# Kernel tuning notes

Measured on AMD Instinct MI355X. Metric: run time of the kernel, lower is better.

Reference implementation:

```python
import jax, jax.numpy as jnp
import numpy as np

EPS = 1e-5          # InstanceNorm eps (torch default)
KERNEL = 25         # moving_avg_kernel_size
TAU = 1.0           # gumbel softmax temperature
REGIME_NUM = 8


def _inorm(x):
    # InstanceNorm1d without affine on (N, C, L): normalize over last dim (biased var)
    m = x.mean(-1, keepdims=True)
    v = ((x - m) ** 2).mean(-1, keepdims=True)
    return (x - m) * jax.lax.rsqrt(v + EPS)


def _lbr(x, W, b):
    # Linear -> InstanceNorm (over last dim) -> exact GELU
    return jax.nn.gelu(_inorm(x @ W + b), approximate=False)


def _moving_avg(x, k):
    # x: (B, L, C); edge-replicate pad (k-1)//2 on both sides, sliding mean via cumsum
    p = (k - 1) // 2
    xp = jnp.concatenate([jnp.repeat(x[:, :1], p, axis=1), x,
                          jnp.repeat(x[:, -1:], p, axis=1)], axis=1)
    cs = jnp.concatenate([jnp.zeros_like(xp[:, :1]), jnp.cumsum(xp, axis=1)], axis=1)
    return (cs[:, k:] - cs[:, :-k]) / k  # (B, L, C)


def _encode(x, Ws, bs, Wt, bt):
    # inputs - inputs[:, 0:1]; series decomposition; seasonal+trend branches
    x = x - x[:, :1]
    mm = _moving_avg(x, KERNEL)
    return _lbr(x - mm, Ws, bs) + _lbr(mm, Wt, bt)  # (B, L, H)


def reference(inputs_longterm, inputs_shortterm,
              Ws, bs, Wt, bt,
              Wh1, bh1, Wl1, bl1, Wh2, bh2, Wl2, bl2, Wh3, bh3, Wl3, bl3,
              Wr, br, proto):
    e_lt = _encode(inputs_longterm, Ws, bs, Wt, bt)   # (B, L_lt, H)
    e_st = _encode(inputs_shortterm, Ws, bs, Wt, bt)  # (B, L_st, H)

    # RegimeEncoder: alternate hidden-dim and lookback-dim LinearBatchRelu layers
    o = _lbr(e_lt, Wh1, bh1)
    o = jnp.swapaxes(_lbr(jnp.swapaxes(o, 1, 2), Wl1, bl1), 1, 2)
    o = _lbr(o, Wh2, bh2)
    o = jnp.swapaxes(_lbr(jnp.swapaxes(o, 1, 2), Wl2, bl2), 1, 2)
    o = _lbr(o, Wh3, bh3)
    o = jnp.swapaxes(_lbr(jnp.swapaxes(o, 1, 2), Wl3, bl3), 1, 2)  # (B, L_lt//8, H)
    logits = o.reshape(o.shape[0], -1) @ Wr + br  # (B, R)

    # gumbel_softmax(hard=True) with straight-through estimator
    g = jax.random.gumbel(jax.random.key(42), logits.shape, logits.dtype)
    y_soft = jax.nn.softmax((logits + g) / TAU, axis=-1)
    y_hard = jax.nn.one_hot(jnp.argmax(y_soft, axis=-1), REGIME_NUM, dtype=logits.dtype)
    w = y_hard - jax.lax.stop_gradient(y_soft) + y_soft  # (B, R)

    # weighted sum over regime prototypes, then combine with encoded shortterm
    sel = jnp.einsum('br,rnhmo->bnhmo', w, proto)          # (B, L_st, H, M, 3)
    out = jnp.einsum('bnh,bnhmo->bmo', e_st, sel)          # (B, M, 3)
    B = out.shape[0]
    return jax.nn.softmax(out.reshape(B, -1), axis=-1).reshape(out.shape)


def setup_inputs() -> dict:
    key = jax.random.key(0)
    ks = jax.random.split(key, 24)
    B, L_lt, L_st, C, H, R, M = 32, 512, 128, 9, 128, 8, 64
    s = 0.02
    d = {
        'inputs_longterm':  jax.random.normal(ks[0], (B, L_lt, C), jnp.float32),
        'inputs_shortterm': jax.random.normal(ks[1], (B, L_st, C), jnp.float32),
        'Ws': jax.random.normal(ks[2], (C, H), jnp.float32) * s,
        'bs': jnp.zeros((H,), jnp.float32),
        'Wt': jax.random.normal(ks[3], (C, H), jnp.float32) * s,
        'bt': jnp.zeros((H,), jnp.float32),
        'Wh1': jax.random.normal(ks[4], (H, H), jnp.float32) * s,
        'bh1': jnp.zeros((H,), jnp.float32),
        'Wl1': jax.random.normal(ks[5], (L_lt, L_lt // 2), jnp.float32) * s,
        'bl1': jnp.zeros((L_lt // 2,), jnp.float32),
        'Wh2': jax.random.normal(ks[6], (H, H), jnp.float32) * s,
        'bh2': jnp.zeros((H,), jnp.float32),
        'Wl2': jax.random.normal(ks[7], (L_lt // 2, L_lt // 4), jnp.float32) * s,
        'bl2': jnp.zeros((L_lt // 4,), jnp.float32),
        'Wh3': jax.random.normal(ks[8], (H, H), jnp.float32) * s,
        'bh3': jnp.zeros((H,), jnp.float32),
        'Wl3': jax.random.normal(ks[9], (L_lt // 4, L_lt // 8), jnp.float32) * s,
        'bl3': jnp.zeros((L_lt // 8,), jnp.float32),
        'Wr': jax.random.normal(ks[10], (H * L_lt // 8, R), jnp.float32) * s,
        'br': jnp.zeros((R,), jnp.float32),
        'proto': jax.random.normal(ks[11], (R, L_st, H, M, 3), jnp.float32),
    }
    return d
```

## Files before the change

### kernel.cpp

```cpp
#include <hip/hip_runtime.h>
#include <math.h>

#define EPS 1e-5f

__device__ __forceinline__ float gelu_exact(float x) {
    return 0.5f * x * (1.0f + erff(x * 0.7071067811865476f));
}

__device__ float block_sum(float v, float* red) {
    int lane = threadIdx.x & 63, wid = threadIdx.x >> 6;
#pragma unroll
    for (int off = 32; off > 0; off >>= 1) v += __shfl_down(v, off, 64);
    if (lane == 0) red[wid] = v;
    __syncthreads();
    int nw = ((int)blockDim.x + 63) >> 6;
    float s = red[0];
    for (int w = 1; w < nw; w++) s += red[w];
    __syncthreads();
    return s;
}

__device__ float block_max(float v, float* red) {
    int lane = threadIdx.x & 63, wid = threadIdx.x >> 6;
#pragma unroll
    for (int off = 32; off > 0; off >>= 1) v = fmaxf(v, __shfl_down(v, off, 64));
    if (lane == 0) red[wid] = v;
    __syncthreads();
    int nw = ((int)blockDim.x + 63) >> 6;
    float s = red[0];
    for (int w = 1; w < nw; w++) s = fmaxf(s, red[w]);
    __syncthreads();
    return s;
}

__device__ void threefry2x32(unsigned k0, unsigned k1, unsigned x0, unsigned x1,
                             unsigned& o0, unsigned& o1) {
    unsigned ks[3] = {k0, k1, k0 ^ k1 ^ 0x1BD11BDAu};
    const unsigned rot[2][4] = {{13u, 15u, 26u, 6u}, {17u, 29u, 16u, 24u}};
    x0 += ks[0]; x1 += ks[1];
#pragma unroll
    for (int i = 0; i < 5; i++) {
#pragma unroll
        for (int j = 0; j < 4; j++) {
            unsigned r = rot[i & 1][j];
            x0 += x1;
            x1 = (x1 << r) | (x1 >> (32 - r));
            x1 ^= x0;
        }
        x0 += ks[(i + 1) % 3];
        x1 += ks[(i + 2) % 3] + (unsigned)(i + 1);
    }
    o0 = x0; o1 = x1;
}

__device__ float gumbel_at(int j) {
    unsigned o0, o1;
    threefry2x32(0u, 42u, 0u, (unsigned)j, o0, o1);
    unsigned bits = o0 ^ o1;
    float f = __uint_as_float((bits >> 9) | 0x3F800000u) - 1.0f;
    float u = fmaxf(f + 1.17549435e-38f, 1.17549435e-38f);
    return -logf(-logf(u));
}

__device__ void bsum2_128(float& a, float& b, float (*red)[2]) {
    int lane = threadIdx.x & 63, wid = threadIdx.x >> 6;
#pragma unroll
    for (int off = 32; off > 0; off >>= 1) {
        a += __shfl_xor(a, off, 64);
        b += __shfl_xor(b, off, 64);
    }
    if (lane == 0) { red[wid][0] = a; red[wid][1] = b; }
    __syncthreads();
    a = red[0][0] + red[1][0];
    b = red[0][1] + red[1][1];
}

__global__ void encode_kernel(const float* __restrict__ x_lt, const float* __restrict__ x_st,
                              const float* __restrict__ Ws, const float* __restrict__ bs,
                              const float* __restrict__ Wt, const float* __restrict__ bt,
                              float* __restrict__ e_lt, float* __restrict__ e_st) {
    const int H = 128;
    int b = blockIdx.y, t = threadIdx.x;
    const float* x;
    float* e;
    int L, l;
    if (blockIdx.x < 512) { x = x_lt; e = e_lt; L = 512; l = blockIdx.x; }
    else { x = x_st; e = e_st; L = 128; l = blockIdx.x - 512; }
    __shared__ float part[117];
    __shared__ float seas[9], mmv[9];
    __shared__ float redA[2][2], redB[2][2];
    const float* xb = x + (size_t)b * L * 9;
    if (t < 117) {
        int c = t / 13, g = t % 13;
        int lj0 = l + 2 * g - 12;
        lj0 = lj0 < 0 ? 0 : (lj0 >= L ? L - 1 : lj0);
        float s = xb[(size_t)lj0 * 9 + c];
        if (g < 12) {
            int lj1 = l + 2 * g - 11;
            lj1 = lj1 < 0 ? 0 : (lj1 >= L ? L - 1 : lj1);
            s += xb[(size_t)lj1 * 9 + c];
        }
        part[t] = s;
    }
    __syncthreads();
    if (t < 9) {
        float s = 0.f;
        for (int g = 0; g < 13; g++) s += part[t * 13 + g];
        float x0 = xb[t];
        float mm = (s - 25.f * x0) * (1.0f / 25.0f);
        float xd = xb[(size_t)l * 9 + t] - x0;
        mmv[t] = mm;
        seas[t] = xd - mm;
    }
    __syncthreads();
    float ys = bs[t], yt = bt[t];
#pragma unroll
    for (int c = 0; c < 9; c++) {
        ys += seas[c] * Ws[c * H + t];
        yt += mmv[c] * Wt[c * H + t];
    }
    float sa = ys, sb = yt;
    bsum2_128(sa, sb, redA);
    float ms = sa * (1.0f / 128.0f), mt = sb * (1.0f / 128.0f);
    float ds = ys - ms, dt = yt - mt;
    float qa = ds * ds, qb = dt * dt;
    bsum2_128(qa, qb, redB);
    float gy = gelu_exact(ds * rsqrtf(qa * (1.0f / 128.0f) + EPS));
    float gt = gelu_exact(dt * rsqrtf(qb * (1.0f / 128.0f) + EPS));
    e[((size_t)b * L + l) * H + t] = gy + gt;
}

template <int K, int N, int WR, bool TRANS>
__global__ __launch_bounds__(256) void lbr_wave(
    const float* __restrict__ A, int S, int ABOFF,
    const float* __restrict__ W, const float* __restrict__ bias,
    float* __restrict__ out, int OROWS, int OBOFF) {
    constexpr int CG = N / 4;
    constexpr int SG = 64 / CG;
    constexpr int RW = SG * WR;
    constexpr int MT = 4 * RW;
    constexpr int LOG2MT = (MT == 8) ? 3 : ((MT == 16) ? 4 : 5);
    constexpr int STAGE = 4 * RW * K;
    constexpr int TILE = TRANS ? MT * (N + 4) : 0;
    constexpr int LSZ = STAGE > TILE ? STAGE : TILE;
    __shared__ float lds[LSZ];
    const int t = threadIdx.x;
    const int w = t >> 6, ln = t & 63;
    const int sg = ln / CG;
    const int n0 = (ln % CG) * 4;
    const int b = blockIdx.y;
    const int r0b = blockIdx.x * MT;
    const int r0w = r0b + w * RW;
    float* As = lds + w * RW * K;
    const float* Ab = A + (size_t)b * ABOFF;
    for (int idx = ln; idx < RW * (K / 4); idx += 64) {
        int rr = idx / (K / 4), kk = idx % (K / 4);
        float4 v = *(const float4*)(Ab + (size_t)(r0w + rr) * S + kk * 4);
        *(float4*)(As + rr * K + kk * 4) = v;
    }
    float4 acc[WR];
    {
        float4 bv = *(const float4*)(bias + n0);
#pragma unroll
        for (int j = 0; j < WR; j++) acc[j] = bv;
    }
    const float* ap = As + (sg * WR) * K;
    const float* wp = W + n0;
#pragma unroll 2
    for (int k = 0; k < K; k += 4) {
        float4 w0 = *(const float4*)(wp);
        float4 w1 = *(const float4*)(wp + N);
        float4 w2 = *(const float4*)(wp + 2 * N);
        float4 w3 = *(const float4*)(wp + 3 * N);
        wp += 4 * N;
#pragma unroll
        for (int j = 0; j < WR; j++) {
            float4 a4 = *(const float4*)(ap + j * K + k);
            acc[j].x += a4.x * w0.x; acc[j].y += a4.x * w0.y;
            acc[j].z += a4.x * w0.z; acc[j].w += a4.x * w0.w;
            acc[j].x += a4.y * w1.x; acc[j].y += a4.y * w1.y;
            acc[j].z += a4.y * w1.z; acc[j].w += a4.y * w1.w;
            acc[j].x += a4.z * w2.x; acc[j].y += a4.z * w2.y;
            acc[j].z += a4.z * w2.z; acc[j].w += a4.z * w2.w;
            acc[j].x += a4.w * w3.x; acc[j].y += a4.w * w3.y;
            acc[j].z += a4.w * w3.z; acc[j].w += a4.w * w3.w;
        }
    }
    float4 res[WR];
#pragma unroll
    for (int j = 0; j < WR; j++) {
        float s = acc[j].x + acc[j].y + acc[j].z + acc[j].w;
#pragma unroll
        for (int off = CG / 2; off > 0; off >>= 1) s += __shfl_xor(s, off, 64);
        float m = s * (1.0f / (float)N);
        float dx = acc[j].x - m, dy = acc[j].y - m, dz = acc[j].z - m, dw = acc[j].w - m;
        float q = dx * dx + dy * dy + dz * dz + dw * dw;
#pragma unroll
        for (int off = CG / 2; off > 0; off >>= 1) q += __shfl_xor(q, off, 64);
        float inv = rsqrtf(q * (1.0f / (float)N) + EPS);
        res[j].x = gelu_exact(dx * inv);
        res[j].y = gelu_exact(dy * inv);
        res[j].z = gelu_exact(dz * inv);
        res[j].w = gelu_exact(dw * inv);
    }
    if constexpr (TRANS) {
        __syncthreads();
#pragma unroll
        for (int j = 0; j < WR; j++) {
            int rl = w * RW + sg * WR + j;
            *(float4*)(lds + rl * (N + 4) + n0) = res[j];
        }
        __syncthreads();
        float* ob = out + (size_t)b * OBOFF + r0b;
        for (int e = t; e < MT * N; e += 256) {
            int r = e & (MT - 1), n = e >> LOG2MT;
            ob[(size_t)n * OROWS + r] = lds[r * (N + 4) + n];
        }
    } else {
        float* ob = out + (size_t)b * OBOFF;
#pragma unroll
        for (int j = 0; j < WR; j++) {
            int row = r0w + sg * WR + j;
            *(float4*)(ob + (size_t)row * N + n0) = res[j];
        }
    }
}

__global__ __launch_bounds__(256) void logits_select(
    const float* __restrict__ O6, const float* __restrict__ Wr,
    const float* __restrict__ br, float* __restrict__ sel_w, int* __restrict__ sel_r) {
    int b = blockIdx.x, t = threadIdx.x;
    __shared__ float sO6[128 * 68];
    __shared__ float red[4][8];
    const float4* ob4 = (const float4*)(O6 + (size_t)b * 8192);
    for (int i4 = t; i4 < 2048; i4 += 256) {
        float4 v = ob4[i4];
        int p = i4 * 4;
        int h = p >> 6, l4 = p & 63;
        *(float4*)(&sO6[h * 68 + l4]) = v;
    }
    __syncthreads();
    float acc[8] = {0, 0, 0, 0, 0, 0, 0, 0};
#pragma unroll 4
    for (int q = 0; q < 32; q++) {
        int i = q * 256 + t;
        int l4 = i >> 7, h = i & 127;
        float v = sO6[h * 68 + l4];
        const float4* wr = (const float4*)(Wr + (size_t)i * 8);
        float4 w0 = wr[0], w1 = wr[1];
        acc[0] += v * w0.x; acc[1] += v * w0.y; acc[2] += v * w0.z; acc[3] += v * w0.w;
        acc[4] += v * w1.x; acc[5] += v * w1.y; acc[6] += v * w1.z; acc[7] += v * w1.w;
    }
#pragma unroll
    for (int j = 0; j < 8; j++)
#pragma unroll
        for (int off = 32; off > 0; off >>= 1) acc[j] += __shfl_xor(acc[j], off, 64);
    int lane = t & 63, wid = t >> 6;
    if (lane == 0)
        for (int j = 0; j < 8; j++) red[wid][j] = acc[j];
    __syncthreads();
    if (t == 0) {
        float z[8];
        for (int j = 0; j < 8; j++) {
            float lg = br[j] + red[0][j] + red[1][j] + red[2][j] + red[3][j];
            z[j] = lg + gumbel_at(b * 8 + j);
        }
        int am = 0;
        float zm = z[0];
        for (int j = 1; j < 8; j++)
            if (z[j] > zm) { zm = z[j]; am = j; }
        float ssum = 0.f;
        for (int j = 0; j < 8; j++) ssum += expf(z[j] - zm);
        float s = 1.0f / ssum;
        sel_w[b] = (1.0f - s) + s;
        sel_r[b] = am;
    }
}

__global__ void einsum_nsplit(const float* __restrict__ e_st, const float* __restrict__ proto,
                              const int* __restrict__ sel_r, float* __restrict__ part) {
    int n = blockIdx.x, r = blockIdx.y, t = threadIdx.x;
    __shared__ int loc[32];
    __shared__ int s_gs;
    if (t == 0) {
        int g = 0;
        for (int bb = 0; bb < 32; bb++)
            if (sel_r[bb] == r) loc[g++] = bb;
        s_gs = g;
    }
    __syncthreads();
    int gs = s_gs;
    if (gs == 0) return;
    __shared__ float es[8][128];
    const float* pb = proto + ((size_t)r * 128 + n) * 128 * 192;
    for (int s0 = 0; s0 < gs; s0 += 8) {
        int np = gs - s0 < 8 ? gs - s0 : 8;
        __syncthreads();
        for (int i4 = t; i4 < 256; i4 += 192) {
            int sb = i4 >> 5, h4 = i4 & 31;
            float4 v = make_float4(0.f, 0.f, 0.f, 0.f);
            if (sb < np) {
                int b = loc[s0 + sb];
                v = ((const float4*)(e_st + ((size_t)b * 128 + n) * 128))[h4];
            }
            *(float4*)(&es[sb][h4 * 4]) = v;
        }
        __syncthreads();
        float a0 = 0.f, a1 = 0.f, a2 = 0.f, a3 = 0.f;
        float a4 = 0.f, a5 = 0.f, a6 = 0.f, a7 = 0.f;
#pragma unroll 8
        for (int h = 0; h < 128; h++) {
            float p = pb[h * 192 + t];
            a0 += es[0][h] * p; a1 += es[1][h] * p;
            a2 += es[2][h] * p; a3 += es[3][h] * p;
            a4 += es[4][h] * p; a5 += es[5][h] * p;
            a6 += es[6][h] * p; a7 += es[7][h] * p;
        }
        float av[8] = {a0, a1, a2, a3, a4, a5, a6, a7};
#pragma unroll
        for (int sb = 0; sb < 8; sb++) {
            if (sb < np) {
                int b = loc[s0 + sb];
                part[((size_t)b * 128 + n) * 192 + t] = av[sb];
            }
        }
    }
}

__global__ void finalize_kernel(const float* __restrict__ part, const float* __restrict__ sel_w,
                                float* __restrict__ out) {
    int b = blockIdx.x, t = threadIdx.x;
    __shared__ float red[4];
    float v = 0.f;
#pragma unroll 8
    for (int c = 0; c < 128; c++) v += part[((size_t)b * 128 + c) * 192 + t];
    v *= sel_w[b];
    float mx = block_max(v, red);
    float e = expf(v - mx);
    float s = block_sum(e, red);
    out[(size_t)b * 192 + t] = e / s;
}

extern "C" void kernel_launch(void* const* d_in, const int* in_sizes, int n_in,
                              void* d_out, int out_size, void* d_ws, size_t ws_size,
                              hipStream_t stream) {
    const float* in_lt = (const float*)d_in[0];
    const float* in_st = (const float*)d_in[1];
    const float* Ws  = (const float*)d_in[2];  const float* bs  = (const float*)d_in[3];
    const float* Wt  = (const float*)d_in[4];  const float* bt  = (const float*)d_in[5];
    const float* Wh1 = (const float*)d_in[6];  const float* bh1 = (const float*)d_in[7];
    const float* Wl1 = (const float*)d_in[8];  const float* bl1 = (const float*)d_in[9];
    const float* Wh2 = (const float*)d_in[10]; const float* bh2 = (const float*)d_in[11];
    const float* Wl2 = (const float*)d_in[12]; const float* bl2 = (const float*)d_in[13];
    const float* Wh3 = (const float*)d_in[14]; const float* bh3 = (const float*)d_in[15];
    const float* Wl3 = (const float*)d_in[16]; const float* bl3 = (const float*)d_in[17];
    const float* Wr  = (const float*)d_in[18]; const float* br  = (const float*)d_in[19];
    const float* proto = (const float*)d_in[20];
    float* out = (float*)d_out;

    float* ws = (float*)d_ws;
    size_t off = 0;
    float* e_lt = ws + off; off += (size_t)32 * 512 * 128;
    float* e_st = ws + off; off += (size_t)32 * 128 * 128;
    float* O1T = ws + off; off += (size_t)128 * 16384;
    float* O2T = ws + off; off += (size_t)256 * 4096;
    float* O3T = ws + off; off += (size_t)128 * 8192;
    float* O4T = ws + off; off += (size_t)128 * 4096;
    float* O5T = ws + off; off += (size_t)128 * 4096;
    float* O6 = ws + off; off += (size_t)32 * 128 * 64;
    float* part = ws + off; off += (size_t)32 * 128 * 192;
    float* sel_w = ws + off; off += 32;
    int* sel_r = (int*)(ws + off); off += 32;

    encode_kernel<<<dim3(640, 32), 128, 0, stream>>>(in_lt, in_st, Ws, bs, Wt, bt, e_lt, e_st);
    lbr_wave<128, 128, 2, true><<<dim3(1024, 1), 256, 0, stream>>>(
        e_lt, 128, 0, Wh1, bh1, O1T, 16384, 0);
    lbr_wave<512, 256, 2, true><<<dim3(16, 32), 256, 0, stream>>>(
        O1T, 16384, 512, Wl1, bl1, O2T, 4096, 128);
    lbr_wave<128, 128, 2, true><<<dim3(16, 32), 256, 0, stream>>>(
        O2T, 4096, 128, Wh2, bh2, O3T, 8192, 256);
    lbr_wave<256, 128, 1, true><<<dim3(16, 32), 256, 0, stream>>>(
        O3T, 8192, 256, Wl2, bl2, O4T, 4096, 128);
    lbr_wave<128, 128, 1, true><<<dim3(16, 32), 256, 0, stream>>>(
        O4T, 4096, 128, Wh3, bh3, O5T, 4096, 128);
    lbr_wave<128, 64, 1, false><<<dim3(8, 32), 256, 0, stream>>>(
        O5T, 4096, 128, Wl3, bl3, O6, 0, 8192);
    logits_select<<<32, 256, 0, stream>>>(O6, Wr, br, sel_w, sel_r);
    einsum_nsplit<<<dim3(128, 8), 192, 0, stream>>>(e_st, proto, sel_r, part);
    finalize_kernel<<<32, 192, 0, stream>>>(part, sel_w, out);
}
```

Baseline: 362.2 us.

## Fuse all stages into one persistent cooperative kernel with grid syncs

Replaces the ten separate kernel launches with a single cooperative persistent kernel of 512 blocks that walks every stage in grid-stride loops and separates stages with grid.sync(). The encode stage is also rewritten so each wave handles one row, using shuffles instead of shared memory and block barriers. The aim is to remove per-launch overhead and the inter-kernel gaps on a pipeline of many small stages. In exchange it adds grid-wide barrier cost, and occupancy is capped by the shared-memory footprint of the largest stage and by launch_bounds(256,2).

```diff
diff --git a/kernel.cpp b/kernel.cpp
--- a/kernel.cpp
+++ b/kernel.cpp
@@ -1,36 +1,13 @@
 #include <hip/hip_runtime.h>
+#include <hip/hip_cooperative_groups.h>
 #include <math.h>
+
+namespace cg = cooperative_groups;
 
 #define EPS 1e-5f
 
 __device__ __forceinline__ float gelu_exact(float x) {
     return 0.5f * x * (1.0f + erff(x * 0.7071067811865476f));
-}
-
-__device__ float block_sum(float v, float* red) {
-    int lane = threadIdx.x & 63, wid = threadIdx.x >> 6;
-#pragma unroll
-    for (int off = 32; off > 0; off >>= 1) v += __shfl_down(v, off, 64);
-    if (lane == 0) red[wid] = v;
-    __syncthreads();
-    int nw = ((int)blockDim.x + 63) >> 6;
-    float s = red[0];
-    for (int w = 1; w < nw; w++) s += red[w];
-    __syncthreads();
-    return s;
-}
-
-__device__ float block_max(float v, float* red) {
-    int lane = threadIdx.x & 63, wid = threadIdx.x >> 6;
-#pragma unroll
-    for (int off = 32; off > 0; off >>= 1) v = fmaxf(v, __shfl_down(v, off, 64));
-    if (lane == 0) red[wid] = v;
-    __syncthreads();
-    int nw = ((int)blockDim.x + 63) >> 6;
-    float s = red[0];
-    for (int w = 1; w < nw; w++) s = fmaxf(s, red[w]);
-    __syncthreads();
-    return s;
 }
 
 __device__ void threefry2x32(unsigned k0, unsigned k1, unsigned x0, unsigned x1,
@@ -62,330 +39,349 @@
     return -logf(-logf(u));
 }
 
-__device__ void bsum2_128(float& a, float& b, float (*red)[2]) {
-    int lane = threadIdx.x & 63, wid = threadIdx.x >> 6;
-#pragma unroll
-    for (int off = 32; off > 0; off >>= 1) {
-        a += __shfl_xor(a, off, 64);
-        b += __shfl_xor(b, off, 64);
-    }
-    if (lane == 0) { red[wid][0] = a; red[wid][1] = b; }
-    __syncthreads();
-    a = red[0][0] + red[1][0];
-    b = red[0][1] + red[1][1];
-}
-
-__global__ void encode_kernel(const float* __restrict__ x_lt, const float* __restrict__ x_st,
-                              const float* __restrict__ Ws, const float* __restrict__ bs,
-                              const float* __restrict__ Wt, const float* __restrict__ bt,
-                              float* __restrict__ e_lt, float* __restrict__ e_st) {
-    const int H = 128;
-    int b = blockIdx.y, t = threadIdx.x;
+struct MegaParams {
+    const float *in_lt, *in_st;
+    const float *Ws, *bs, *Wt, *bt;
+    const float *Wh1, *bh1, *Wl1, *bl1, *Wh2, *bh2, *Wl2, *bl2;
+    const float *Wh3, *bh3, *Wl3, *bl3, *Wr, *br, *proto;
+    float* out;
+    float *e_lt, *e_st, *O1T, *O2T, *O3T, *O4T, *O5T, *O6, *part, *sel_w;
+    int* sel_r;
+};
+
+__device__ void encode_row_wave(int task, const MegaParams& p, int ln) {
     const float* x;
     float* e;
-    int L, l;
-    if (blockIdx.x < 512) { x = x_lt; e = e_lt; L = 512; l = blockIdx.x; }
-    else { x = x_st; e = e_st; L = 128; l = blockIdx.x - 512; }
-    __shared__ float part[117];
-    __shared__ float seas[9], mmv[9];
-    __shared__ float redA[2][2], redB[2][2];
+    int L, b, l;
+    if (task < 16384) { x = p.in_lt; e = p.e_lt; L = 512; b = task >> 9; l = task & 511; }
+    else { int u = task - 16384; x = p.in_st; e = p.e_st; L = 128; b = u >> 7; l = u & 127; }
     const float* xb = x + (size_t)b * L * 9;
-    if (t < 117) {
-        int c = t / 13, g = t % 13;
-        int lj0 = l + 2 * g - 12;
-        lj0 = lj0 < 0 ? 0 : (lj0 >= L ? L - 1 : lj0);
-        float s = xb[(size_t)lj0 * 9 + c];
-        if (g < 12) {
-            int lj1 = l + 2 * g - 11;
-            lj1 = lj1 < 0 ? 0 : (lj1 >= L ? L - 1 : lj1);
-            s += xb[(size_t)lj1 * 9 + c];
-        }
-        part[t] = s;
-    }
-    __syncthreads();
-    if (t < 9) {
+    float seas_v = 0.f, mm_v = 0.f;
+    if (ln < 9) {
+        float x0 = xb[ln];
         float s = 0.f;
-        for (int g = 0; g < 13; g++) s += part[t * 13 + g];
-        float x0 = xb[t];
+#pragma unroll
+        for (int j = -12; j <= 12; j++) {
+            int lj = l + j;
+            lj = lj < 0 ? 0 : (lj >= L ? L - 1 : lj);
+            s += xb[(size_t)lj * 9 + ln];
+        }
         float mm = (s - 25.f * x0) * (1.0f / 25.0f);
-        float xd = xb[(size_t)l * 9 + t] - x0;
-        mmv[t] = mm;
-        seas[t] = xd - mm;
-    }
-    __syncthreads();
-    float ys = bs[t], yt = bt[t];
+        mm_v = mm;
+        seas_v = (xb[(size_t)l * 9 + ln] - x0) - mm;
+    }
+    int h1 = ln, h2 = ln + 64;
+    float ys1 = p.bs[h1], ys2 = p.bs[h2], yt1 = p.bt[h1], yt2 = p.bt[h2];
 #pragma unroll
     for (int c = 0; c < 9; c++) {
-        ys += seas[c] * Ws[c * H + t];
-        yt += mmv[c] * Wt[c * H + t];
-    }
-    float sa = ys, sb = yt;
-    bsum2_128(sa, sb, redA);
+        float sc = __shfl(seas_v, c, 64);
+        float mc = __shfl(mm_v, c, 64);
+        ys1 += sc * p.Ws[c * 128 + h1]; ys2 += sc * p.Ws[c * 128 + h2];
+        yt1 += mc * p.Wt[c * 128 + h1]; yt2 += mc * p.Wt[c * 128 + h2];
+    }
+    float sa = ys1 + ys2, sb = yt1 + yt2;
+#pragma unroll
+    for (int off = 32; off > 0; off >>= 1) {
+        sa += __shfl_xor(sa, off, 64);
+        sb += __shfl_xor(sb, off, 64);
+    }
     float ms = sa * (1.0f / 128.0f), mt = sb * (1.0f / 128.0f);
-    float ds = ys - ms, dt = yt - mt;
-    float qa = ds * ds, qb = dt * dt;
-    bsum2_128(qa, qb, redB);
-    float gy = gelu_exact(ds * rsqrtf(qa * (1.0f / 128.0f) + EPS));
-    float gt = gelu_exact(dt * rsqrtf(qb * (1.0f / 128.0f) + EPS));
-    e[((size_t)b * L + l) * H + t] = gy + gt;
+    float d1 = ys1 - ms, d2 = ys2 - ms, f1 = yt1 - mt, f2 = yt2 - mt;
+    float qa = d1 * d1 + d2 * d2, qb = f1 * f1 + f2 * f2;
+#pragma unroll
+    for (int off = 32; off > 0; off >>= 1) {
+        qa += __shfl_xor(qa, off, 64);
+        qb += __shfl_xor(qb, off, 64);
+    }
+    float is = rsqrtf(qa * (1.0f / 128.0f) + EPS);
+    float it = rsqrtf(qb * (1.0f / 128.0f) + EPS);
+    float o1 = gelu_exact(d1 * is) + gelu_exact(f1 * it);
+    float o2 = gelu_exact(d2 * is) + gelu_exact(f2 * it);
+    float* eb = e + ((size_t)b * L + l) * 128;
+    eb[h1] = o1;
+    eb[h2] = o2;
 }
 
 template <int K, int N, int WR, bool TRANS>
-__global__ __launch_bounds__(256) void lbr_wave(
-    const float* __restrict__ A, int S, int ABOFF,
-    const float* __restrict__ W, const float* __restrict__ bias,
-    float* __restrict__ out, int OROWS, int OBOFF) {
+__device__ void layer_phase(float* lds,
+                            const float* __restrict__ A, int S, int ABOFF,
+                            const float* __restrict__ W, const float* __restrict__ bias,
+                            float* __restrict__ out, int OROWS, int OBOFF,
+                            int tilesX, int nB) {
     constexpr int CG = N / 4;
     constexpr int SG = 64 / CG;
     constexpr int RW = SG * WR;
     constexpr int MT = 4 * RW;
     constexpr int LOG2MT = (MT == 8) ? 3 : ((MT == 16) ? 4 : 5);
-    constexpr int STAGE = 4 * RW * K;
-    constexpr int TILE = TRANS ? MT * (N + 4) : 0;
-    constexpr int LSZ = STAGE > TILE ? STAGE : TILE;
-    __shared__ float lds[LSZ];
     const int t = threadIdx.x;
     const int w = t >> 6, ln = t & 63;
     const int sg = ln / CG;
     const int n0 = (ln % CG) * 4;
-    const int b = blockIdx.y;
-    const int r0b = blockIdx.x * MT;
-    const int r0w = r0b + w * RW;
-    float* As = lds + w * RW * K;
-    const float* Ab = A + (size_t)b * ABOFF;
-    for (int idx = ln; idx < RW * (K / 4); idx += 64) {
-        int rr = idx / (K / 4), kk = idx % (K / 4);
-        float4 v = *(const float4*)(Ab + (size_t)(r0w + rr) * S + kk * 4);
-        *(float4*)(As + rr * K + kk * 4) = v;
-    }
-    float4 acc[WR];
-    {
-        float4 bv = *(const float4*)(bias + n0);
-#pragma unroll
-        for (int j = 0; j < WR; j++) acc[j] = bv;
-    }
-    const float* ap = As + (sg * WR) * K;
-    const float* wp = W + n0;
+    const int ntask = tilesX * nB;
+    for (int tt = blockIdx.x; tt < ntask; tt += gridDim.x) {
+        const int bx = tt % tilesX, b = tt / tilesX;
+        const int r0b = bx * MT;
+        const int r0w = r0b + w * RW;
+        float* As = lds + w * RW * K;
+        const float* Ab = A + (size_t)b * ABOFF;
+        for (int idx = ln; idx < RW * (K / 4); idx += 64) {
+            int rr = idx / (K / 4), kk = idx % (K / 4);
+            float4 v = *(const float4*)(Ab + (size_t)(r0w + rr) * S + kk * 4);
+            *(float4*)(As + rr * K + kk * 4) = v;
+        }
+        float4 acc[WR];
+        {
+            float4 bv = *(const float4*)(bias + n0);
+#pragma unroll
+            for (int j = 0; j < WR; j++) acc[j] = bv;
+        }
+        const float* ap = As + (sg * WR) * K;
+        const float* wp = W + n0;
 #pragma unroll 2
-    for (int k = 0; k < K; k += 4) {
-        float4 w0 = *(const float4*)(wp);
-        float4 w1 = *(const float4*)(wp + N);
-        float4 w2 = *(const float4*)(wp + 2 * N);
-        float4 w3 = *(const float4*)(wp + 3 * N);
-        wp += 4 * N;
+        for (int k = 0; k < K; k += 4) {
+            float4 w0 = *(const float4*)(wp);
+            float4 w1 = *(const float4*)(wp + N);
+            float4 w2 = *(const float4*)(wp + 2 * N);
+            float4 w3 = *(const float4*)(wp + 3 * N);
+            wp += 4 * N;
+#pragma unroll
+            for (int j = 0; j < WR; j++) {
+                float4 a4 = *(const float4*)(ap + j * K + k);
+                acc[j].x += a4.x * w0.x; acc[j].y += a4.x * w0.y;
+                acc[j].z += a4.x * w0.z; acc[j].w += a4.x * w0.w;
+                acc[j].x += a4.y * w1.x; acc[j].y += a4.y * w1.y;
+                acc[j].z += a4.y * w1.z; acc[j].w += a4.y * w1.w;
+                acc[j].x += a4.z * w2.x; acc[j].y += a4.z * w2.y;
+                acc[j].z += a4.z * w2.z; acc[j].w += a4.z * w2.w;
+                acc[j].x += a4.w * w3.x; acc[j].y += a4.w * w3.y;
+                acc[j].z += a4.w * w3.z; acc[j].w += a4.w * w3.w;
+            }
+        }
+        float4 res[WR];
 #pragma unroll
         for (int j = 0; j < WR; j++) {
-            float4 a4 = *(const float4*)(ap + j * K + k);
-            acc[j].x += a4.x * w0.x; acc[j].y += a4.x * w0.y;
-            acc[j].z += a4.x * w0.z; acc[j].w += a4.x * w0.w;
-            acc[j].x += a4.y * w1.x; acc[j].y += a4.y * w1.y;
-            acc[j].z += a4.y * w1.z; acc[j].w += a4.y * w1.w;
-            acc[j].x += a4.z * w2.x; acc[j].y += a4.z * w2.y;
-            acc[j].z += a4.z * w2.z; acc[j].w += a4.z * w2.w;
-            acc[j].x += a4.w * w3.x; acc[j].y += a4.w * w3.y;
-            acc[j].z += a4.w * w3.z; acc[j].w += a4.w * w3.w;
-        }
-    }
-    float4 res[WR];
-#pragma unroll
-    for (int j = 0; j < WR; j++) {
-        float s = acc[j].x + acc[j].y + acc[j].z + acc[j].w;
-#pragma unroll
-        for (int off = CG / 2; off > 0; off >>= 1) s += __shfl_xor(s, off, 64);
-        float m = s * (1.0f / (float)N);
-        float dx = acc[j].x - m, dy = acc[j].y - m, dz = acc[j].z - m, dw = acc[j].w - m;
-        float q = dx * dx + dy * dy + dz * dz + dw * dw;
-#pragma unroll
-        for (int off = CG / 2; off > 0; off >>= 1) q += __shfl_xor(q, off, 64);
-        float inv = rsqrtf(q * (1.0f / (float)N) + EPS);
-        res[j].x = gelu_exact(dx * inv);
-        res[j].y = gelu_exact(dy * inv);
-        res[j].z = gelu_exact(dz * inv);
-        res[j].w = gelu_exact(dw * inv);
-    }
-    if constexpr (TRANS) {
-        __syncthreads();
-#pragma unroll
-        for (int j = 0; j < WR; j++) {
-            int rl = w * RW + sg * WR + j;
-            *(float4*)(lds + rl * (N + 4) + n0) = res[j];
-        }
-        __syncthreads();
-        float* ob = out + (size_t)b * OBOFF + r0b;
-        for (int e = t; e < MT * N; e += 256) {
-            int r = e & (MT - 1), n = e >> LOG2MT;
-            ob[(size_t)n * OROWS + r] = lds[r * (N + 4) + n];
-        }
-    } else {
-        float* ob = out + (size_t)b * OBOFF;
-#pragma unroll
-        for (int j = 0; j < WR; j++) {
-            int row = r0w + sg * WR + j;
-            *(float4*)(ob + (size_t)row * N + n0) = res[j];
-        }
-    }
-}
-
-__global__ __launch_bounds__(256) void logits_select(
-    const float* __restrict__ O6, const float* __restrict__ Wr,
-    const float* __restrict__ br, float* __restrict__ sel_w, int* __restrict__ sel_r) {
-    int b = blockIdx.x, t = threadIdx.x;
-    __shared__ float sO6[128 * 68];
-    __shared__ float red[4][8];
-    const float4* ob4 = (const float4*)(O6 + (size_t)b * 8192);
-    for (int i4 = t; i4 < 2048; i4 += 256) {
-        float4 v = ob4[i4];
-        int p = i4 * 4;
-        int h = p >> 6, l4 = p & 63;
-        *(float4*)(&sO6[h * 68 + l4]) = v;
-    }
-    __syncthreads();
-    float acc[8] = {0, 0, 0, 0, 0, 0, 0, 0};
-#pragma unroll 4
-    for (int q = 0; q < 32; q++) {
-        int i = q * 256 + t;
-        int l4 = i >> 7, h = i & 127;
-        float v = sO6[h * 68 + l4];
-        const float4* wr = (const float4*)(Wr + (size_t)i * 8);
-        float4 w0 = wr[0], w1 = wr[1];
-        acc[0] += v * w0.x; acc[1] += v * w0.y; acc[2] += v * w0.z; acc[3] += v * w0.w;
-        acc[4] += v * w1.x; acc[5] += v * w1.y; acc[6] += v * w1.z; acc[7] += v * w1.w;
-    }
-#pragma unroll
-    for (int j = 0; j < 8; j++)
-#pragma unroll
-        for (int off = 32; off > 0; off >>= 1) acc[j] += __shfl_xor(acc[j], off, 64);
-    int lane = t & 63, wid = t >> 6;
-    if (lane == 0)
-        for (int j = 0; j < 8; j++) red[wid][j] = acc[j];
-    __syncthreads();
-    if (t == 0) {
-        float z[8];
-        for (int j = 0; j < 8; j++) {
-            float lg = br[j] + red[0][j] + red[1][j] + red[2][j] + red[3][j];
-            z[j] = lg + gumbel_at(b * 8 + j);
-        }
-        int am = 0;
-        float zm = z[0];
-        for (int j = 1; j < 8; j++)
-            if (z[j] > zm) { zm = z[j]; am = j; }
-        float ssum = 0.f;
-        for (int j = 0; j < 8; j++) ssum += expf(z[j] - zm);
-        float s = 1.0f / ssum;
-        sel_w[b] = (1.0f - s) + s;
-        sel_r[b] = am;
-    }
-}
-
-__global__ void einsum_nsplit(const float* __restrict__ e_st, const float* __restrict__ proto,
-                              const int* __restrict__ sel_r, float* __restrict__ part) {
-    int n = blockIdx.x, r = blockIdx.y, t = threadIdx.x;
+            float s = acc[j].x + acc[j].y + acc[j].z + acc[j].w;
+#pragma unroll
+            for (int off = CG / 2; off > 0; off >>= 1) s += __shfl_xor(s, off, 64);
+            float m = s * (1.0f / (float)N);
+            float dx = acc[j].x - m, dy = acc[j].y - m, dz = acc[j].z - m, dw = acc[j].w - m;
+            float q = dx * dx + dy * dy + dz * dz + dw * dw;
+#pragma unroll
+            for (int off = CG / 2; off > 0; off >>= 1) q += __shfl_xor(q, off, 64);
+            float inv = rsqrtf(q * (1.0f / (float)N) + EPS);
+            res[j].x = gelu_exact(dx * inv);
+            res[j].y = gelu_exact(dy * inv);
+            res[j].z = gelu_exact(dz * inv);
+            res[j].w = gelu_exact(dw * inv);
+        }
+        if constexpr (TRANS) {
+            __syncthreads();
+#pragma unroll
+            for (int j = 0; j < WR; j++) {
+                int rl = w * RW + sg * WR + j;
+                *(float4*)(lds + rl * (N + 4) + n0) = res[j];
+            }
+            __syncthreads();
+            float* ob = out + (size_t)b * OBOFF + r0b;
+            for (int e2 = t; e2 < MT * N; e2 += 256) {
+                int r = e2 & (MT - 1), n = e2 >> LOG2MT;
+                ob[(size_t)n * OROWS + r] = lds[r * (N + 4) + n];
+            }
+            __syncthreads();
+        } else {
+            float* ob = out + (size_t)b * OBOFF;
+#pragma unroll
+            for (int j = 0; j < WR; j++) {
+                int row = r0w + sg * WR + j;
+                *(float4*)(ob + (size_t)row * N + n0) = res[j];
+            }
+        }
+    }
+}
+
+__global__ __launch_bounds__(256, 2) void mega(MegaParams p) {
+    cg::grid_group grid = cg::this_grid();
+    __shared__ float lds[8704];
+    __shared__ float red8[4][8];
     __shared__ int loc[32];
     __shared__ int s_gs;
-    if (t == 0) {
-        int g = 0;
-        for (int bb = 0; bb < 32; bb++)
-            if (sel_r[bb] == r) loc[g++] = bb;
-        s_gs = g;
-    }
-    __syncthreads();
-    int gs = s_gs;
-    if (gs == 0) return;
-    __shared__ float es[8][128];
-    const float* pb = proto + ((size_t)r * 128 + n) * 128 * 192;
-    for (int s0 = 0; s0 < gs; s0 += 8) {
-        int np = gs - s0 < 8 ? gs - s0 : 8;
-        __syncthreads();
-        for (int i4 = t; i4 < 256; i4 += 192) {
-            int sb = i4 >> 5, h4 = i4 & 31;
-            float4 v = make_float4(0.f, 0.f, 0.f, 0.f);
-            if (sb < np) {
-                int b = loc[s0 + sb];
-                v = ((const float4*)(e_st + ((size_t)b * 128 + n) * 128))[h4];
-            }
-            *(float4*)(&es[sb][h4 * 4]) = v;
-        }
-        __syncthreads();
-        float a0 = 0.f, a1 = 0.f, a2 = 0.f, a3 = 0.f;
-        float a4 = 0.f, a5 = 0.f, a6 = 0.f, a7 = 0.f;
+    const int t = threadIdx.x;
+    const int w = t >> 6, ln = t & 63;
+    const int blk = blockIdx.x, nblk = gridDim.x;
+    const int gw = blk * 4 + w;
+    const int ngw = nblk * 4;
+
+    for (int task = gw; task < 20480; task += ngw) encode_row_wave(task, p, ln);
+    grid.sync();
+    layer_phase<128, 128, 2, true>(lds, p.e_lt, 128, 0, p.Wh1, p.bh1, p.O1T, 16384, 0, 1024, 1);
+    grid.sync();
+    layer_phase<512, 256, 2, true>(lds, p.O1T, 16384, 512, p.Wl1, p.bl1, p.O2T, 4096, 128, 16, 32);
+    grid.sync();
+    layer_phase<128, 128, 2, true>(lds, p.O2T, 4096, 128, p.Wh2, p.bh2, p.O3T, 8192, 256, 16, 32);
+    grid.sync();
+    layer_phase<256, 128, 1, true>(lds, p.O3T, 8192, 256, p.Wl2, p.bl2, p.O4T, 4096, 128, 16, 32);
+    grid.sync();
+    layer_phase<128, 128, 1, true>(lds, p.O4T, 4096, 128, p.Wh3, p.bh3, p.O5T, 4096, 128, 16, 32);
+    grid.sync();
+    layer_phase<128, 64, 1, false>(lds, p.O5T, 4096, 128, p.Wl3, p.bl3, p.O6, 0, 8192, 8, 32);
+    grid.sync();
+
+    for (int b = blk; b < 32; b += nblk) {
+        const float4* ob4 = (const float4*)(p.O6 + (size_t)b * 8192);
+        for (int i4 = t; i4 < 2048; i4 += 256) {
+            float4 v = ob4[i4];
+            int pidx = i4 * 4;
+            int h = pidx >> 6, l4 = pidx & 63;
+            *(float4*)(&lds[h * 68 + l4]) = v;
+        }
+        __syncthreads();
+        float acc[8] = {0, 0, 0, 0, 0, 0, 0, 0};
+#pragma unroll 4
+        for (int q = 0; q < 32; q++) {
+            int i = q * 256 + t;
+            int l4 = i >> 7, h = i & 127;
+            float v = lds[h * 68 + l4];
+            const float4* wr = (const float4*)(p.Wr + (size_t)i * 8);
+            float4 w0 = wr[0], w1 = wr[1];
+            acc[0] += v * w0.x; acc[1] += v * w0.y; acc[2] += v * w0.z; acc[3] += v * w0.w;
+            acc[4] += v * w1.x; acc[5] += v * w1.y; acc[6] += v * w1.z; acc[7] += v * w1.w;
+        }
+#pragma unroll
+        for (int j = 0; j < 8; j++)
+#pragma unroll
+            for (int off = 32; off > 0; off >>= 1) acc[j] += __shfl_xor(acc[j], off, 64);
+        if (ln == 0)
+            for (int j = 0; j < 8; j++) red8[w][j] = acc[j];
+        __syncthreads();
+        if (t == 0) {
+            float z[8];
+            for (int j = 0; j < 8; j++) {
+                float lg = p.br[j] + red8[0][j] + red8[1][j] + red8[2][j] + red8[3][j];
+                z[j] = lg + gumbel_at(b * 8 + j);
+            }
+            int am = 0;
+            float zm = z[0];
+            for (int j = 1; j < 8; j++)
+                if (z[j] > zm) { zm = z[j]; am = j; }
+            float ssum = 0.f;
+            for (int j = 0; j < 8; j++) ssum += expf(z[j] - zm);
+            float s = 1.0f / ssum;
+            p.sel_w[b] = (1.0f - s) + s;
+            p.sel_r[b] = am;
+        }
+        __syncthreads();
+    }
+    grid.sync();
+
+    for (int task = blk; task < 1024; task += nblk) {
+        int n = task & 127, r = task >> 7;
+        if (t == 0) {
+            int g = 0;
+            for (int bb = 0; bb < 32; bb++)
+                if (p.sel_r[bb] == r) loc[g++] = bb;
+            s_gs = g;
+        }
+        __syncthreads();
+        int gs = s_gs;
+        if (gs != 0) {
+            float* es = lds;
+            const float* pb = p.proto + ((size_t)r * 128 + n) * 128 * 192;
+            for (int s0 = 0; s0 < gs; s0 += 8) {
+                int np = gs - s0 < 8 ? gs - s0 : 8;
+                {
+                    int sb = t >> 5, h4 = t & 31;
+                    float4 v = make_float4(0.f, 0.f, 0.f, 0.f);
+                    if (sb < np) {
+                        int b = loc[s0 + sb];
+                        v = ((const float4*)(p.e_st + ((size_t)b * 128 + n) * 128))[h4];
+                    }
+                    *(float4*)(&es[sb * 128 + h4 * 4]) = v;
+                }
+                __syncthreads();
+                if (t < 192) {
+                    float a0 = 0.f, a1 = 0.f, a2 = 0.f, a3 = 0.f;
+                    float a4 = 0.f, a5 = 0.f, a6 = 0.f, a7 = 0.f;
 #pragma unroll 8
-        for (int h = 0; h < 128; h++) {
-            float p = pb[h * 192 + t];
-            a0 += es[0][h] * p; a1 += es[1][h] * p;
-            a2 += es[2][h] * p; a3 += es[3][h] * p;
-            a4 += es[4][h] * p; a5 += es[5][h] * p;
-            a6 += es[6][h] * p; a7 += es[7][h] * p;
-        }
-        float av[8] = {a0, a1, a2, a3, a4, a5, a6, a7};
-#pragma unroll
-        for (int sb = 0; sb < 8; sb++) {
-            if (sb < np) {
-                int b = loc[s0 + sb];
-                part[((size_t)b * 128 + n) * 192 + t] = av[sb];
-            }
-        }
-    }
-}
-
-__global__ void finalize_kernel(const float* __restrict__ part, const float* __restrict__ sel_w,
-                                float* __restrict__ out) {
-    int b = blockIdx.x, t = threadIdx.x;
-    __shared__ float red[4];
-    float v = 0.f;
+                    for (int h = 0; h < 128; h++) {
+                        float pv = pb[h * 192 + t];
+                        a0 += es[0 * 128 + h] * pv; a1 += es[1 * 128 + h] * pv;
+                        a2 += es[2 * 128 + h] * pv; a3 += es[3 * 128 + h] * pv;
+                        a4 += es[4 * 128 + h] * pv; a5 += es[5 * 128 + h] * pv;
+                        a6 += es[6 * 128 + h] * pv; a7 += es[7 * 128 + h] * pv;
+                    }
+                    float av[8] = {a0, a1, a2, a3, a4, a5, a6, a7};
+#pragma unroll
+                    for (int sb = 0; sb < 8; sb++) {
+                        if (sb < np) {
+                            int b = loc[s0 + sb];
+                            p.part[((size_t)b * 128 + n) * 192 + t] = av[sb];
+                        }
+                    }
+                }
+                __syncthreads();
+            }
+        }
+        __syncthreads();
+    }
+    grid.sync();
+
+    for (int b = blk; b < 32; b += nblk) {
+        float v = 0.f;
+        if (t < 192) {
 #pragma unroll 8
-    for (int c = 0; c < 128; c++) v += part[((size_t)b * 128 + c) * 192 + t];
-    v *= sel_w[b];
-    float mx = block_max(v, red);
-    float e = expf(v - mx);
-    float s = block_sum(e, red);
-    out[(size_t)b * 192 + t] = e / s;
+            for (int c = 0; c < 128; c++) v += p.part[((size_t)b * 128 + c) * 192 + t];
+            v *= p.sel_w[b];
+        }
+        float mv = (t < 192) ? v : -3.402823466e+38f;
+#pragma unroll
+        for (int off = 32; off > 0; off >>= 1) mv = fmaxf(mv, __shfl_xor(mv, off, 64));
+        if (ln == 0) red8[w][0] = mv;
+        __syncthreads();
+        float mx = fmaxf(fmaxf(red8[0][0], red8[1][0]), fmaxf(red8[2][0], red8[3][0]));
+        float e = (t < 192) ? expf(v - mx) : 0.f;
+        float se = e;
+#pragma unroll
+        for (int off = 32; off > 0; off >>= 1) se += __shfl_xor(se, off, 64);
+        __syncthreads();
+        if (ln == 0) red8[w][1] = se;
+        __syncthreads();
+        float s = red8[0][1] + red8[1][1] + red8[2][1] + red8[3][1];
+        if (t < 192) p.out[(size_t)b * 192 + t] = e / s;
+        __syncthreads();
+    }
 }
 
 extern "C" void kernel_launch(void* const* d_in, const int* in_sizes, int n_in,
                               void* d_out, int out_size, void* d_ws, size_t ws_size,
                               hipStream_t stream) {
-    const float* in_lt = (const float*)d_in[0];
-    const float* in_st = (const float*)d_in[1];
-    const float* Ws  = (const float*)d_in[2];  const float* bs  = (const float*)d_in[3];
-    const float* Wt  = (const float*)d_in[4];  const float* bt  = (const float*)d_in[5];
-    const float* Wh1 = (const float*)d_in[6];  const float* bh1 = (const float*)d_in[7];
-    const float* Wl1 = (const float*)d_in[8];  const float* bl1 = (const float*)d_in[9];
-    const float* Wh2 = (const float*)d_in[10]; const float* bh2 = (const float*)d_in[11];
-    const float* Wl2 = (const float*)d_in[12]; const float* bl2 = (const float*)d_in[13];
-    const float* Wh3 = (const float*)d_in[14]; const float* bh3 = (const float*)d_in[15];
-    const float* Wl3 = (const float*)d_in[16]; const float* bl3 = (const float*)d_in[17];
-    const float* Wr  = (const float*)d_in[18]; const float* br  = (const float*)d_in[19];
-    const float* proto = (const float*)d_in[20];
-    float* out = (float*)d_out;
-
     float* ws = (float*)d_ws;
     size_t off = 0;
-    float* e_lt = ws + off; off += (size_t)32 * 512 * 128;
-    float* e_st = ws + off; off += (size_t)32 * 128 * 128;
-    float* O1T = ws + off; off += (size_t)128 * 16384;
-    float* O2T = ws + off; off += (size_t)256 * 4096;
-    float* O3T = ws + off; off += (size_t)128 * 8192;
-    float* O4T = ws + off; off += (size_t)128 * 4096;
-    float* O5T = ws + off; off += (size_t)128 * 4096;
-    float* O6 = ws + off; off += (size_t)32 * 128 * 64;
-    float* part = ws + off; off += (size_t)32 * 128 * 192;
-    float* sel_w = ws + off; off += 32;
-    int* sel_r = (int*)(ws + off); off += 32;
-
-    encode_kernel<<<dim3(640, 32), 128, 0, stream>>>(in_lt, in_st, Ws, bs, Wt, bt, e_lt, e_st);
-    lbr_wave<128, 128, 2, true><<<dim3(1024, 1), 256, 0, stream>>>(
-        e_lt, 128, 0, Wh1, bh1, O1T, 16384, 0);
-    lbr_wave<512, 256, 2, true><<<dim3(16, 32), 256, 0, stream>>>(
-        O1T, 16384, 512, Wl1, bl1, O2T, 4096, 128);
-    lbr_wave<128, 128, 2, true><<<dim3(16, 32), 256, 0, stream>>>(
-        O2T, 4096, 128, Wh2, bh2, O3T, 8192, 256);
-    lbr_wave<256, 128, 1, true><<<dim3(16, 32), 256, 0, stream>>>(
-        O3T, 8192, 256, Wl2, bl2, O4T, 4096, 128);
-    lbr_wave<128, 128, 1, true><<<dim3(16, 32), 256, 0, stream>>>(
-        O4T, 4096, 128, Wh3, bh3, O5T, 4096, 128);
-    lbr_wave<128, 64, 1, false><<<dim3(8, 32), 256, 0, stream>>>(
-        O5T, 4096, 128, Wl3, bl3, O6, 0, 8192);
-    logits_select<<<32, 256, 0, stream>>>(O6, Wr, br, sel_w, sel_r);
-    einsum_nsplit<<<dim3(128, 8), 192, 0, stream>>>(e_st, proto, sel_r, part);
-    finalize_kernel<<<32, 192, 0, stream>>>(part, sel_w, out);
-}
+    MegaParams p;
+    p.in_lt = (const float*)d_in[0];
+    p.in_st = (const float*)d_in[1];
+    p.Ws = (const float*)d_in[2];  p.bs = (const float*)d_in[3];
+    p.Wt = (const float*)d_in[4];  p.bt = (const float*)d_in[5];
+    p.Wh1 = (const float*)d_in[6]; p.bh1 = (const float*)d_in[7];
+    p.Wl1 = (const float*)d_in[8]; p.bl1 = (const float*)d_in[9];
+    p.Wh2 = (const float*)d_in[10]; p.bh2 = (const float*)d_in[11];
+    p.Wl2 = (const float*)d_in[12]; p.bl2 = (const float*)d_in[13];
+    p.Wh3 = (const float*)d_in[14]; p.bh3 = (const float*)d_in[15];
+    p.Wl3 = (const float*)d_in[16]; p.bl3 = (const float*)d_in[17];
+    p.Wr = (const float*)d_in[18]; p.br = (const float*)d_in[19];
+    p.proto = (const float*)d_in[20];
+    p.out = (float*)d_out;
+    p.e_lt = ws + off; off += (size_t)32 * 512 * 128;
+    p.e_st = ws + off; off += (size_t)32 * 128 * 128;
+    p.O1T = ws + off; off += (size_t)128 * 16384;
+    p.O2T = ws + off; off += (size_t)256 * 4096;
+    p.O3T = ws + off; off += (size_t)128 * 8192;
+    p.O4T = ws + off; off += (size_t)128 * 4096;
+    p.O5T = ws + off; off += (size_t)128 * 4096;
+    p.O6 = ws + off; off += (size_t)32 * 128 * 64;
+    p.part = ws + off; off += (size_t)32 * 128 * 192;
+    p.sel_w = ws + off; off += 32;
+    p.sel_r = (int*)(ws + off); off += 32;
+
+    void* kp[] = {&p};
+    hipLaunchCooperativeKernel((const void*)mega, dim3(512), dim3(256), kp, 0, stream);
+}
```

Result: slower. 1.000 ms (+176.2%).

## Fuse series-decomposition encoder into first hidden-dim LBR kernel

Applied to the files above, without the earlier changes.

The encoder for the long-term input is now computed inside the first LinearBatchRelu kernel, with one wave per row, and the result goes straight to shared memory instead of through a global e_lt buffer. The encoder itself is rewritten to use wave shuffles instead of block-level shared reductions and syncs. Extra blocks in the same launch handle the short-term encoding. The aim is to cut one launch and a 8MB round trip through global memory. The cost is a serial 25-tap moving average per row inside the GEMM kernel, which may lengthen the per-block critical path.

```diff
diff --git a/kernel.cpp b/kernel.cpp
--- a/kernel.cpp
+++ b/kernel.cpp
@@ -62,72 +62,137 @@
     return -logf(-logf(u));
 }
 
-__device__ void bsum2_128(float& a, float& b, float (*red)[2]) {
-    int lane = threadIdx.x & 63, wid = threadIdx.x >> 6;
+__device__ float2 encode_row(const float* __restrict__ xb, int L, int l, int ln,
+                             const float* __restrict__ Ws, const float* __restrict__ bs,
+                             const float* __restrict__ Wt, const float* __restrict__ bt) {
+    float seas_v = 0.f, mm_v = 0.f;
+    if (ln < 9) {
+        float x0 = xb[ln];
+        float s = 0.f;
+#pragma unroll
+        for (int j = -12; j <= 12; j++) {
+            int lj = l + j;
+            lj = lj < 0 ? 0 : (lj >= L ? L - 1 : lj);
+            s += xb[(size_t)lj * 9 + ln];
+        }
+        float mm = (s - 25.f * x0) * (1.0f / 25.0f);
+        mm_v = mm;
+        seas_v = (xb[(size_t)l * 9 + ln] - x0) - mm;
+    }
+    int h1 = ln, h2 = ln + 64;
+    float ys1 = bs[h1], ys2 = bs[h2], yt1 = bt[h1], yt2 = bt[h2];
+#pragma unroll
+    for (int c = 0; c < 9; c++) {
+        float sc = __shfl(seas_v, c, 64);
+        float mc = __shfl(mm_v, c, 64);
+        ys1 += sc * Ws[c * 128 + h1]; ys2 += sc * Ws[c * 128 + h2];
+        yt1 += mc * Wt[c * 128 + h1]; yt2 += mc * Wt[c * 128 + h2];
+    }
+    float sa = ys1 + ys2, sb = yt1 + yt2;
 #pragma unroll
     for (int off = 32; off > 0; off >>= 1) {
-        a += __shfl_xor(a, off, 64);
-        b += __shfl_xor(b, off, 64);
-    }
-    if (lane == 0) { red[wid][0] = a; red[wid][1] = b; }
-    __syncthreads();
-    a = red[0][0] + red[1][0];
-    b = red[0][1] + red[1][1];
-}
-
-__global__ void encode_kernel(const float* __restrict__ x_lt, const float* __restrict__ x_st,
-                              const float* __restrict__ Ws, const float* __restrict__ bs,
-                              const float* __restrict__ Wt, const float* __restrict__ bt,
-                              float* __restrict__ e_lt, float* __restrict__ e_st) {
-    const int H = 128;
-    int b = blockIdx.y, t = threadIdx.x;
-    const float* x;
-    float* e;
-    int L, l;
-    if (blockIdx.x < 512) { x = x_lt; e = e_lt; L = 512; l = blockIdx.x; }
-    else { x = x_st; e = e_st; L = 128; l = blockIdx.x - 512; }
-    __shared__ float part[117];
-    __shared__ float seas[9], mmv[9];
-    __shared__ float redA[2][2], redB[2][2];
-    const float* xb = x + (size_t)b * L * 9;
-    if (t < 117) {
-        int c = t / 13, g = t % 13;
-        int lj0 = l + 2 * g - 12;
-        lj0 = lj0 < 0 ? 0 : (lj0 >= L ? L - 1 : lj0);
-        float s = xb[(size_t)lj0 * 9 + c];
-        if (g < 12) {
-            int lj1 = l + 2 * g - 11;
-            lj1 = lj1 < 0 ? 0 : (lj1 >= L ? L - 1 : lj1);
-            s += xb[(size_t)lj1 * 9 + c];
-        }
-        part[t] = s;
-    }
-    __syncthreads();
-    if (t < 9) {
-        float s = 0.f;
-        for (int g = 0; g < 13; g++) s += part[t * 13 + g];
-        float x0 = xb[t];
-        float mm = (s - 25.f * x0) * (1.0f / 25.0f);
-        float xd = xb[(size_t)l * 9 + t] - x0;
-        mmv[t] = mm;
-        seas[t] = xd - mm;
-    }
-    __syncthreads();
-    float ys = bs[t], yt = bt[t];
-#pragma unroll
-    for (int c = 0; c < 9; c++) {
-        ys += seas[c] * Ws[c * H + t];
-        yt += mmv[c] * Wt[c * H + t];
-    }
-    float sa = ys, sb = yt;
-    bsum2_128(sa, sb, redA);
+        sa += __shfl_xor(sa, off, 64);
+        sb += __shfl_xor(sb, off, 64);
+    }
     float ms = sa * (1.0f / 128.0f), mt = sb * (1.0f / 128.0f);
-    float ds = ys - ms, dt = yt - mt;
-    float qa = ds * ds, qb = dt * dt;
-    bsum2_128(qa, qb, redB);
-    float gy = gelu_exact(ds * rsqrtf(qa * (1.0f / 128.0f) + EPS));
-    float gt = gelu_exact(dt * rsqrtf(qb * (1.0f / 128.0f) + EPS));
-    e[((size_t)b * L + l) * H + t] = gy + gt;
+    float d1 = ys1 - ms, d2 = ys2 - ms, f1 = yt1 - mt, f2 = yt2 - mt;
+    float qa = d1 * d1 + d2 * d2, qb = f1 * f1 + f2 * f2;
+#pragma unroll
+    for (int off = 32; off > 0; off >>= 1) {
+        qa += __shfl_xor(qa, off, 64);
+        qb += __shfl_xor(qb, off, 64);
+    }
+    float is = rsqrtf(qa * (1.0f / 128.0f) + EPS);
+    float it = rsqrtf(qb * (1.0f / 128.0f) + EPS);
+    return make_float2(gelu_exact(d1 * is) + gelu_exact(f1 * it),
+                       gelu_exact(d2 * is) + gelu_exact(f2 * it));
+}
+
+__global__ __launch_bounds__(256) void h1_enc(
+    const float* __restrict__ in_lt, const float* __restrict__ in_st,
+    const float* __restrict__ Ws, const float* __restrict__ bs,
+    const float* __restrict__ Wt, const float* __restrict__ bt,
+    const float* __restrict__ W, const float* __restrict__ bias,
+    float* __restrict__ O1T, float* __restrict__ e_st) {
+    const int t = threadIdx.x, w = t >> 6, ln = t & 63;
+    const int blk = blockIdx.x;
+    if (blk < 1024) {
+        __shared__ float lds[2112];
+        const int sg = ln >> 5;
+        const int n0 = (ln & 31) * 4;
+        const int r0b = blk * 16, r0w = r0b + w * 4;
+        float* As = lds + w * 512;
+        for (int rr = 0; rr < 4; rr++) {
+            int row = r0w + rr, bb = row >> 9, l = row & 511;
+            float2 o = encode_row(in_lt + (size_t)bb * 4608, 512, l, ln, Ws, bs, Wt, bt);
+            As[rr * 128 + ln] = o.x;
+            As[rr * 128 + ln + 64] = o.y;
+        }
+        float4 acc[2];
+        {
+            float4 bv = *(const float4*)(bias + n0);
+            acc[0] = bv; acc[1] = bv;
+        }
+        const float* ap = As + (sg * 2) * 128;
+        const float* wp = W + n0;
+#pragma unroll 2
+        for (int k = 0; k < 128; k += 4) {
+            float4 w0 = *(const float4*)(wp);
+            float4 w1 = *(const float4*)(wp + 128);
+            float4 w2 = *(const float4*)(wp + 256);
+            float4 w3 = *(const float4*)(wp + 384);
+            wp += 512;
+#pragma unroll
+            for (int j = 0; j < 2; j++) {
+                float4 a4 = *(const float4*)(ap + j * 128 + k);
+                acc[j].x += a4.x * w0.x; acc[j].y += a4.x * w0.y;
+                acc[j].z += a4.x * w0.z; acc[j].w += a4.x * w0.w;
+                acc[j].x += a4.y * w1.x; acc[j].y += a4.y * w1.y;
+                acc[j].z += a4.y * w1.z; acc[j].w += a4.y * w1.w;
+                acc[j].x += a4.z * w2.x; acc[j].y += a4.z * w2.y;
+                acc[j].z += a4.z * w2.z; acc[j].w += a4.z * w2.w;
+                acc[j].x += a4.w * w3.x; acc[j].y += a4.w * w3.y;
+                acc[j].z += a4.w * w3.z; acc[j].w += a4.w * w3.w;
+            }
+        }
+        float4 res[2];
+#pragma unroll
+        for (int j = 0; j < 2; j++) {
+            float s = acc[j].x + acc[j].y + acc[j].z + acc[j].w;
+#pragma unroll
+            for (int off = 16; off > 0; off >>= 1) s += __shfl_xor(s, off, 64);
+            float m = s * (1.0f / 128.0f);
+            float dx = acc[j].x - m, dy = acc[j].y - m, dz = acc[j].z - m, dw = acc[j].w - m;
+            float q = dx * dx + dy * dy + dz * dz + dw * dw;
+#pragma unroll
+            for (int off = 16; off > 0; off >>= 1) q += __shfl_xor(q, off, 64);
+            float inv = rsqrtf(q * (1.0f / 128.0f) + EPS);
+            res[j].x = gelu_exact(dx * inv);
+            res[j].y = gelu_exact(dy * inv);
+            res[j].z = gelu_exact(dz * inv);
+            res[j].w = gelu_exact(dw * inv);
+        }
+        __syncthreads();
+#pragma unroll
+        for (int j = 0; j < 2; j++) {
+            int rl = w * 4 + sg * 2 + j;
+            *(float4*)(lds + rl * 132 + n0) = res[j];
+        }
+        __syncthreads();
+        float* ob = O1T + r0b;
+        for (int e2 = t; e2 < 16 * 128; e2 += 256) {
+            int r = e2 & 15, n = e2 >> 4;
+            ob[(size_t)n * 16384 + r] = lds[r * 132 + n];
+        }
+    } else {
+        for (int row = (blk - 1024) * 4 + w; row < 4096; row += 256) {
+            int b = row >> 7, l = row & 127;
+            float2 o = encode_row(in_st + (size_t)b * 1152, 128, l, ln, Ws, bs, Wt, bt);
+            float* eb = e_st + (size_t)row * 128;
+            eb[ln] = o.x;
+            eb[ln + 64] = o.y;
+        }
+    }
 }
 
 template <int K, int N, int WR, bool TRANS>
@@ -360,7 +425,6 @@
 
     float* ws = (float*)d_ws;
     size_t off = 0;
-    float* e_lt = ws + off; off += (size_t)32 * 512 * 128;
     float* e_st = ws + off; off += (size_t)32 * 128 * 128;
     float* O1T = ws + off; off += (size_t)128 * 16384;
     float* O2T = ws + off; off += (size_t)256 * 4096;
@@ -372,9 +436,7 @@
     float* sel_w = ws + off; off += 32;
     int* sel_r = (int*)(ws + off); off += 32;
 
-    encode_kernel<<<dim3(640, 32), 128, 0, stream>>>(in_lt, in_st, Ws, bs, Wt, bt, e_lt, e_st);
-    lbr_wave<128, 128, 2, true><<<dim3(1024, 1), 256, 0, stream>>>(
-        e_lt, 128, 0, Wh1, bh1, O1T, 16384, 0);
+    h1_enc<<<1088, 256, 0, stream>>>(in_lt, in_st, Ws, bs, Wt, bt, Wh1, bh1, O1T, e_st);
     lbr_wave<512, 256, 2, true><<<dim3(16, 32), 256, 0, stream>>>(
         O1T, 16384, 512, Wl1, bl1, O2T, 4096, 128);
     lbr_wave<128, 128, 2, true><<<dim3(16, 32), 256, 0, stream>>>(
```

New measurement: 384.0 us. 6.0% more time.
